# Optimization experiments

Hardware: AMD Instinct MI355X
Metric: run time of the kernel (lower is better)

The kernel has to match this reference:

```python
import jax, jax.numpy as jnp
import numpy as np

B, W, F = 16384, 64, 120
EPS = 1e-3  # keras BatchNormalization default epsilon


def _bn(x, g, b, m, v):
    return g * (x - m) * jax.lax.rsqrt(v + EPS) + b


def setup_inputs() -> dict:
    key = jax.random.key(0)
    ks = jax.random.split(key, 32)
    n = lambda i, s: jax.random.normal(ks[i], s, dtype=jnp.float32) * 0.05
    u = lambda i, s: jax.random.uniform(ks[i], s, dtype=jnp.float32) + 0.5
    W3 = W * 3
    return {
        'x': jax.random.normal(ks[0], (B, W, F), dtype=jnp.float32),
        # per-timestep Conv1D: only center tap matters on length-1 seq -> [W, F, 3]
        'conv_w': n(1, (W, F, 3)), 'conv_b': n(2, (W, 3)),
        # eye head
        'e_g1': u(3, (W3,)), 'e_b1': n(4, (W3,)), 'e_m1': n(5, (W3,)), 'e_v1': u(6, (W3,)),
        'e_d1_w': n(7, (W3, W3)), 'e_d1_b': n(8, (W3,)),
        'e_g2': u(9, (W3,)), 'e_b2': n(10, (W3,)), 'e_m2': n(11, (W3,)), 'e_v2': u(12, (W3,)),
        'e_d2_w': n(13, (W3, 2 * F)), 'e_d2_b': n(14, (2 * F,)),
        'e_d3_w': n(15, (2 * F, F)), 'e_d3_b': n(16, (F,)),
        # blink head
        'b_g1': u(17, (W3,)), 'b_b1': n(18, (W3,)), 'b_m1': n(19, (W3,)), 'b_v1': u(20, (W3,)),
        'b_d1_w': n(21, (W3, W)), 'b_d1_b': n(22, (W,)),
        'b_g2': u(23, (W,)), 'b_b2': n(24, (W,)), 'b_m2': n(25, (W,)), 'b_v2': u(26, (W,)),
        'b_d2_w': n(27, (W, W // 2)), 'b_d2_b': n(28, (W // 2,)),
        'b_d3_w': n(29, (W // 2, 1)), 'b_d3_b': n(30, (1,)),
    }


def reference(x, conv_w, conv_b, e_g1, e_b1, e_m1, e_v1, e_d1_w, e_d1_b,
              e_g2, e_b2, e_m2, e_v2, e_d2_w, e_d2_b, e_d3_w, e_d3_b,
              b_g1, b_b1, b_m1, b_v1, b_d1_w, b_d1_b,
              b_g2, b_b2, b_m2, b_v2, b_d2_w, b_d2_b, b_d3_w, b_d3_b):
    # window_size independent Conv1D(k=3,'same') on length-1 sequences reduce to a
    # single batched per-timestep matmul with the center kernel tap.
    combined = jnp.tanh(jnp.einsum('bwf,wfk->bwk', x, conv_w) + conv_b)
    combined = combined.reshape(x.shape[0], -1)  # [B, 3*W]
    # eye-feature head (dropout = identity at inference, BN uses moving stats)
    e = _bn(combined, e_g1, e_b1, e_m1, e_v1)
    e = jnp.tanh(e @ e_d1_w + e_d1_b)
    e = _bn(e, e_g2, e_b2, e_m2, e_v2)
    e = e @ e_d2_w + e_d2_b
    e = e @ e_d3_w + e_d3_b  # [B, F]
    # blink head
    b = _bn(combined, b_g1, b_b1, b_m1, b_v1)
    b = jnp.tanh(b @ b_d1_w + b_d1_b)
    b = _bn(b, b_g2, b_b2, b_m2, b_v2)
    b = jnp.tanh(b @ b_d2_w + b_d2_b)
    b = jax.nn.sigmoid(b @ b_d3_w + b_d3_b)  # [B, 1]
    return jnp.concatenate([e, b], axis=-1)  # [B, F+1]
```

## Files before the change

kernel.cpp:

```cpp
#include <hip/hip_runtime.h>
#include <hip/hip_bf16.h>
#include <string.h>

#define EPSBN 1e-3f

constexpr int kC1  = 192;
constexpr int kN2  = 240;
constexpr int kOut = 121;
constexpr int BTOT = 16384;

typedef __attribute__((ext_vector_type(8))) short bf16x8;
typedef __attribute__((ext_vector_type(4))) float f32x4;

__device__ __forceinline__ unsigned short f2bf(float f) {
  union { float f; unsigned u; } v; v.f = f;
  unsigned r = v.u + 0x7FFFu + ((v.u >> 16) & 1u);
  return (unsigned short)(r >> 16);
}
__device__ __forceinline__ float bf2f(unsigned short h) {
  union { unsigned u; float f; } v; v.u = ((unsigned)h) << 16;
  return v.f;
}

constexpr size_t OFF_W1E  = 0;
constexpr size_t OFF_W2E  = OFF_W1E + 73728;
constexpr size_t OFF_W3E  = OFF_W2E + 92160;
constexpr size_t OFF_W1B  = OFF_W3E + 65536;
constexpr size_t OFF_W2B  = OFF_W1B + 24576;
constexpr size_t OFF_BIAS = OFF_W2B + 4096;
constexpr size_t OFF_CWT  = OFF_BIAS + 2736;
constexpr size_t WS_NEED  = OFF_CWT + 122880;

__device__ __forceinline__ void pack_one(unsigned short* dst, int idx,
                                         const float* __restrict__ W, int Ksrc, int Nsrc,
                                         int KS, const float* g, const float* v)
{
  int per_nt = KS * 512;
  int nt = idx / per_nt; int r = idx - nt * per_nt;
  int ks = r >> 9; int r2 = r & 511;
  int l = r2 >> 3; int j = r2 & 7;
  int i = ks * 32 + ((l >> 4) << 3) + j;
  int n = (nt << 4) + (l & 15);
  float val = 0.f;
  if (i < Ksrc && n < Nsrc) {
    float s = g ? g[i] * rsqrtf(v[i] + EPSBN) : 1.f;
    val = s * W[(size_t)i * Nsrc + n];
  }
  dst[idx] = f2bf(val);
}

__device__ __forceinline__ float wave_dot192(const float* g, const float* b,
                                             const float* m, const float* vv,
                                             const float* W, int Nsrc, int j, int lane)
{
  float p = 0.f;
  #pragma unroll
  for (int t = 0; t < 3; ++t) {
    int i = t * 64 + lane;
    float s = g[i] * rsqrtf(vv[i] + EPSBN);
    p = fmaf(b[i] - m[i] * s, W[(size_t)i * Nsrc + j], p);
  }
  #pragma unroll
  for (int o = 32; o > 0; o >>= 1) p += __shfl_xor(p, o);
  return p;
}

__global__ __launch_bounds__(256) void prep_all(
    const float* conv_w,
    const float* e_g1, const float* e_b1, const float* e_m1, const float* e_v1,
    const float* e_d1_w, const float* e_d1_b,
    const float* e_g2, const float* e_b2, const float* e_m2, const float* e_v2,
    const float* e_d2_w, const float* e_d2_b,
    const float* e_d3_w, const float* e_d3_b,
    const float* b_g1, const float* b_b1, const float* b_m1, const float* b_v1,
    const float* b_d1_w, const float* b_d1_b,
    const float* b_g2, const float* b_b2, const float* b_m2, const float* b_v2,
    const float* b_d2_w, const float* b_d2_b,
    const float* b_d3_w, const float* b_d3_b,
    unsigned short* W1E, unsigned short* W2E, unsigned short* W3E,
    unsigned short* W1B, unsigned short* W2B,
    float* BIAS, float* cwt4)
{
  const int b   = blockIdx.x;
  const int tid = threadIdx.x;

  if (b < 508) {
    int e = b * 256 + tid;
    if (e < 36864)               pack_one(W1E, e,          e_d1_w, 192, 192, 6, e_g1, e_v1);
    else if (e < 82944)          pack_one(W2E, e - 36864,  e_d2_w, 192, 240, 6, e_g2, e_v2);
    else if (e < 115712)         pack_one(W3E, e - 82944,  e_d3_w, 240, 120, 8, nullptr, nullptr);
    else if (e < 128000)         pack_one(W1B, e - 115712, b_d1_w, 192, 64,  6, b_g1, b_v1);
    else if (e < 130048)         pack_one(W2B, e - 128000, b_d2_w, 64,  32,  2, b_g2, b_v2);
  } else if (b < 538) {
    int idx = (b - 508) * 256 + tid;
    if (idx < 7680) {
      int f = idx >> 6, w = idx & 63;
      float4 v;
      v.x = conv_w[(size_t)w * 360 + f * 3 + 0];
      v.y = conv_w[(size_t)w * 360 + f * 3 + 1];
      v.z = conv_w[(size_t)w * 360 + f * 3 + 2];
      v.w = 0.f;
      *reinterpret_cast<float4*>(cwt4 + (size_t)idx * 4) = v;
    }
  } else {
    int lane = tid & 63;
    int q = (b - 538) * 4 + (tid >> 6);
    if (q > 680) return;
    float r;
    if (q < 192) {
      r = wave_dot192(e_g1, e_b1, e_m1, e_v1, e_d1_w, 192, q, lane) + e_d1_b[q];
    } else if (q < 432) {
      int j = q - 192;
      r = wave_dot192(e_g2, e_b2, e_m2, e_v2, e_d2_w, 240, j, lane) + e_d2_b[j];
    } else if (q < 552) {
      r = e_d3_b[q - 432];
    } else if (q < 616) {
      int j = q - 552;
      r = wave_dot192(b_g1, b_b1, b_m1, b_v1, b_d1_w, 64, j, lane) + b_d1_b[j];
    } else if (q < 648) {
      int j = q - 616;
      float s = b_g2[lane] * rsqrtf(b_v2[lane] + EPSBN);
      float p = (b_b2[lane] - b_m2[lane] * s) * b_d2_w[(size_t)lane * 32 + j];
      #pragma unroll
      for (int o = 32; o > 0; o >>= 1) p += __shfl_xor(p, o);
      r = p + b_d2_b[j];
    } else if (q < 680) {
      r = b_d3_w[q - 648];
    } else {
      r = b_d3_b[0];
    }
    if (lane == 0) BIAS[q] = r;
  }
}

__global__ __launch_bounds__(64) void fused_all(
    const float* __restrict__ x,
    const float* __restrict__ cwt4, const float* __restrict__ conv_b,
    const unsigned short* __restrict__ W1E, const unsigned short* __restrict__ W2E,
    const unsigned short* __restrict__ W3E, const unsigned short* __restrict__ W1B,
    const unsigned short* __restrict__ W2B, const float* __restrict__ BIAS,
    float* __restrict__ out)
{
  __shared__ __align__(16) short Ac[16 * 200];
  __shared__ __align__(16) char  ubuf[15 * 65 * 16];

  float4* xt = reinterpret_cast<float4*>(ubuf);
  short*  Hs = reinterpret_cast<short*>(ubuf);
  short*  H2 = reinterpret_cast<short*>(ubuf + 6400);

  const int l = threadIdx.x;
  const int R = blockIdx.x * 16;

  {
    const float bc0 = conv_b[l * 3 + 0];
    const float bc1 = conv_b[l * 3 + 1];
    const float bc2 = conv_b[l * 3 + 2];

    for (int r = 0; r < 16; ++r) {
      const float* xrow = x + (size_t)(R + r) * 7680;
      float a0 = 0.f, a1 = 0.f, a2 = 0.f;

      for (int h = 0; h < 2; ++h) {
        #pragma unroll
        for (int i = 0; i < 15; ++i) {
          int g = i * 64 + l;
          int w = g / 15, fs = g - 15 * w;
          float4 v = *reinterpret_cast<const float4*>(xrow + w * 120 + h * 60 + 4 * fs);
          xt[fs * 65 + w] = v;
        }
        __syncthreads();

        #pragma unroll 5
        for (int fq = 0; fq < 15; ++fq) {
          float4 x4 = xt[fq * 65 + l];
          float xs[4] = {x4.x, x4.y, x4.z, x4.w};
          #pragma unroll
          for (int j = 0; j < 4; ++j) {
            int f = h * 60 + 4 * fq + j;
            float4 c4 = *reinterpret_cast<const float4*>(cwt4 + (size_t)(f * 64 + l) * 4);
            a0 = fmaf(xs[j], c4.x, a0);
            a1 = fmaf(xs[j], c4.y, a1);
            a2 = fmaf(xs[j], c4.z, a2);
          }
        }
        __syncthreads();
      }

      Ac[r * 200 + 3 * l + 0] = (short)f2bf(tanhf(a0 + bc0));
      Ac[r * 200 + 3 * l + 1] = (short)f2bf(tanhf(a1 + bc1));
      Ac[r * 200 + 3 * l + 2] = (short)f2bf(tanhf(a2 + bc2));
    }
  }
  __syncthreads();

  #pragma unroll
  for (int e = l; e < 256; e += 64) {
    int row = e >> 4, cc = e & 15;
    H2[row * 264 + 240 + cc] = 0;
  }

  const int arow = l & 15;
  const int kofs = (l >> 4) * 8;
  const int mb   = (l >> 4) * 4;

  for (int nt = 0; nt < 12; ++nt) {
    f32x4 acc = {0.f, 0.f, 0.f, 0.f};
    const bf16x8* bp = (const bf16x8*)W1E + (size_t)(nt * 6) * 64 + l;
    #pragma unroll
    for (int ks = 0; ks < 6; ++ks) {
      bf16x8 a = *(const bf16x8*)(Ac + arow * 200 + ks * 32 + kofs);
      acc = __builtin_amdgcn_mfma_f32_16x16x32_bf16(a, bp[(size_t)ks * 64], acc, 0, 0, 0);
    }
    int n = nt * 16 + arow;
    float bv = BIAS[n];
    __syncthreads();
    #pragma unroll
    for (int r = 0; r < 4; ++r)
      Hs[(mb + r) * 200 + n] = (short)f2bf(tanhf(acc[r] + bv));
  }
  __syncthreads();

  for (int nt = 0; nt < 15; ++nt) {
    f32x4 acc = {0.f, 0.f, 0.f, 0.f};
    const bf16x8* bp = (const bf16x8*)W2E + (size_t)(nt * 6) * 64 + l;
    #pragma unroll
    for (int ks = 0; ks < 6; ++ks) {
      bf16x8 a = *(const bf16x8*)(Hs + arow * 200 + ks * 32 + kofs);
      acc = __builtin_amdgcn_mfma_f32_16x16x32_bf16(a, bp[(size_t)ks * 64], acc, 0, 0, 0);
    }
    int n = nt * 16 + arow;
    float bv = BIAS[192 + n];
    #pragma unroll
    for (int r = 0; r < 4; ++r)
      H2[(mb + r) * 264 + n] = (short)f2bf(acc[r] + bv);
  }
  __syncthreads();

  for (int nt = 0; nt < 8; ++nt) {
    f32x4 acc = {0.f, 0.f, 0.f, 0.f};
    const bf16x8* bp = (const bf16x8*)W3E + (size_t)(nt * 8) * 64 + l;
    #pragma unroll
    for (int ks = 0; ks < 8; ++ks) {
      bf16x8 a = *(const bf16x8*)(H2 + arow * 264 + ks * 32 + kofs);
      acc = __builtin_amdgcn_mfma_f32_16x16x32_bf16(a, bp[(size_t)ks * 64], acc, 0, 0, 0);
    }
    int n = nt * 16 + arow;
    if (n < 120) {
      float bv = BIAS[432 + n];
      #pragma unroll
      for (int r = 0; r < 4; ++r)
        out[(size_t)(R + mb + r) * kOut + n] = acc[r] + bv;
    }
  }
  __syncthreads();

  for (int nt = 0; nt < 4; ++nt) {
    f32x4 acc = {0.f, 0.f, 0.f, 0.f};
    const bf16x8* bp = (const bf16x8*)W1B + (size_t)(nt * 6) * 64 + l;
    #pragma unroll
    for (int ks = 0; ks < 6; ++ks) {
      bf16x8 a = *(const bf16x8*)(Ac + arow * 200 + ks * 32 + kofs);
      acc = __builtin_amdgcn_mfma_f32_16x16x32_bf16(a, bp[(size_t)ks * 64], acc, 0, 0, 0);
    }
    int n = nt * 16 + arow;
    float bv = BIAS[552 + n];
    #pragma unroll
    for (int r = 0; r < 4; ++r)
      Hs[(mb + r) * 200 + n] = (short)f2bf(tanhf(acc[r] + bv));
  }
  __syncthreads();

  for (int nt = 0; nt < 2; ++nt) {
    f32x4 acc = {0.f, 0.f, 0.f, 0.f};
    const bf16x8* bp = (const bf16x8*)W2B + (size_t)(nt * 2) * 64 + l;
    #pragma unroll
    for (int ks = 0; ks < 2; ++ks) {
      bf16x8 a = *(const bf16x8*)(Hs + arow * 200 + ks * 32 + kofs);
      acc = __builtin_amdgcn_mfma_f32_16x16x32_bf16(a, bp[(size_t)ks * 64], acc, 0, 0, 0);
    }
    int n = nt * 16 + arow;
    float bv = BIAS[616 + n];
    #pragma unroll
    for (int r = 0; r < 4; ++r)
      H2[(mb + r) * 264 + n] = (short)f2bf(tanhf(acc[r] + bv));
  }
  __syncthreads();

  if (l < 16) {
    float s = BIAS[680];
    #pragma unroll
    for (int i = 0; i < 32; ++i)
      s = fmaf(bf2f((unsigned short)H2[l * 264 + i]), BIAS[648 + i], s);
    out[(size_t)(R + l) * kOut + 120] = 1.f / (1.f + expf(-s));
  }
}

constexpr int CSTR = 193;
__global__ __launch_bounds__(64, 4) void fused_blink_fb(
    const float* __restrict__ x,
    const float* __restrict__ conv_w, const float* __restrict__ conv_b,
    const float* __restrict__ e_g1, const float* __restrict__ e_b1,
    const float* __restrict__ e_m1, const float* __restrict__ e_v1,
    const float* __restrict__ e_d1_w, const float* __restrict__ e_d1_b,
    const float* __restrict__ e_g2, const float* __restrict__ e_b2,
    const float* __restrict__ e_m2, const float* __restrict__ e_v2,
    const float* __restrict__ e_d2_w, const float* __restrict__ e_d2_b,
    const float* __restrict__ e_d3_w, const float* __restrict__ e_d3_b,
    const float* __restrict__ b_g1, const float* __restrict__ b_b1,
    const float* __restrict__ b_m1, const float* __restrict__ b_v1,
    const float* __restrict__ b_d1_w, const float* __restrict__ b_d1_b,
    const float* __restrict__ b_g2, const float* __restrict__ b_b2,
    const float* __restrict__ b_m2, const float* __restrict__ b_v2,
    const float* __restrict__ b_d2_w, const float* __restrict__ b_d2_b,
    const float* __restrict__ b_d3_w, const float* __restrict__ b_d3_b,
    float* __restrict__ out)
{
  __shared__ float comb[4 * CSTR];
  __shared__ __align__(16) float Ab[4 * kN2];
  __shared__ __align__(16) float Bb[4 * kN2];
  const int lane = threadIdx.x;
  const int b0   = blockIdx.x * 4;
  {
    const int rcv = lane >> 4, wloc = lane & 15;
    for (int wc = 0; wc < 4; ++wc) {
      const int w = wc * 16 + wloc;
      const float* xr  = x + ((size_t)(b0 + rcv) * 64 + w) * 120;
      const float* cwp = conv_w + (size_t)w * 360;
      float a0 = 0.f, a1 = 0.f, a2 = 0.f;
      for (int t = 0; t < 30; ++t) {
        float4 xv = *reinterpret_cast<const float4*>(xr + 4 * t);
        float4 c0 = *reinterpret_cast<const float4*>(cwp + 12 * t);
        float4 c1 = *reinterpret_cast<const float4*>(cwp + 12 * t + 4);
        float4 c2 = *reinterpret_cast<const float4*>(cwp + 12 * t + 8);
        a0 += xv.x * c0.x + xv.y * c0.w + xv.z * c1.z + xv.w * c2.y;
        a1 += xv.x * c0.y + xv.y * c1.x + xv.z * c1.w + xv.w * c2.z;
        a2 += xv.x * c0.z + xv.y * c1.y + xv.z * c2.x + xv.w * c2.w;
      }
      comb[rcv * CSTR + 3 * w + 0] = tanhf(a0 + conv_b[3 * w + 0]);
      comb[rcv * CSTR + 3 * w + 1] = tanhf(a1 + conv_b[3 * w + 1]);
      comb[rcv * CSTR + 3 * w + 2] = tanhf(a2 + conv_b[3 * w + 2]);
    }
  }
  __syncthreads();
  #define AR(rr) (Ab + (size_t)(rr) * kN2)
  #define BR(rr) (Bb + (size_t)(rr) * kN2)
  #pragma unroll
  for (int q = 0; q < 12; ++q) {
    int rr = q / 3, cc = q % 3;
    int i = cc * 64 + lane;
    float s = e_g1[i] * rsqrtf(e_v1[i] + EPSBN);
    AR(rr)[i] = comb[rr * CSTR + i] * s + (e_b1[i] - e_m1[i] * s);
  }
  __syncthreads();
  {
    float acc[4][3];
    #pragma unroll
    for (int rr = 0; rr < 4; ++rr) { acc[rr][0]=acc[rr][1]=acc[rr][2]=0.f; }
    for (int i = 0; i < kC1; i += 4) {
      float4 v[4];
      #pragma unroll
      for (int rr = 0; rr < 4; ++rr) v[rr] = *reinterpret_cast<const float4*>(AR(rr) + i);
      #pragma unroll
      for (int io = 0; io < 4; ++io) {
        const float* wp = e_d1_w + (size_t)(i + io) * kC1 + lane;
        float w0 = wp[0], w1 = wp[64], w2 = wp[128];
        #pragma unroll
        for (int rr = 0; rr < 4; ++rr) {
          float xv = reinterpret_cast<const float*>(&v[rr])[io];
          acc[rr][0] = fmaf(xv, w0, acc[rr][0]);
          acc[rr][1] = fmaf(xv, w1, acc[rr][1]);
          acc[rr][2] = fmaf(xv, w2, acc[rr][2]);
        }
      }
    }
    #pragma unroll
    for (int c = 0; c < 3; ++c) {
      int j = c * 64 + lane;
      float s  = e_g2[j] * rsqrtf(e_v2[j] + EPSBN);
      float t  = e_b2[j] - e_m2[j] * s;
      float bs = e_d1_b[j];
      #pragma unroll
      for (int rr = 0; rr < 4; ++rr)
        BR(rr)[j] = tanhf(acc[rr][c] + bs) * s + t;
    }
  }
  __syncthreads();
  {
    const bool m3 = (lane < 48);
    float acc[4][4];
    #pragma unroll
    for (int rr = 0; rr < 4; ++rr) { acc[rr][0]=acc[rr][1]=acc[rr][2]=acc[rr][3]=0.f; }
    for (int i = 0; i < kC1; i += 4) {
      float4 v[4];
      #pragma unroll
      for (int rr = 0; rr < 4; ++rr) v[rr] = *reinterpret_cast<const float4*>(BR(rr) + i);
      #pragma unroll
      for (int io = 0; io < 4; ++io) {
        const float* wp = e_d2_w + (size_t)(i + io) * kN2 + lane;
        float w0 = wp[0], w1 = wp[64], w2 = wp[128];
        float w3 = m3 ? wp[192] : 0.f;
        #pragma unroll
        for (int rr = 0; rr < 4; ++rr) {
          float xv = reinterpret_cast<const float*>(&v[rr])[io];
          acc[rr][0] = fmaf(xv, w0, acc[rr][0]);
          acc[rr][1] = fmaf(xv, w1, acc[rr][1]);
          acc[rr][2] = fmaf(xv, w2, acc[rr][2]);
          acc[rr][3] = fmaf(xv, w3, acc[rr][3]);
        }
      }
    }
    #pragma unroll
    for (int c = 0; c < 4; ++c) {
      int j = c * 64 + lane;
      if (c < 3 || m3) {
        float bs = e_d2_b[j];
        #pragma unroll
        for (int rr = 0; rr < 4; ++rr)
          AR(rr)[j] = acc[rr][c] + bs;
      }
    }
  }
  __syncthreads();
  #pragma unroll
  for (int q = 0; q < 12; ++q) {
    int rr = q / 3, cc = q % 3;
    int i = cc * 64 + lane;
    float s = b_g1[i] * rsqrtf(b_v1[i] + EPSBN);
    BR(rr)[i] = comb[rr * CSTR + i] * s + (b_b1[i] - b_m1[i] * s);
  }
  {
    const bool m56 = (lane < 56);
    float acc[4][2];
    #pragma unroll
    for (int rr = 0; rr < 4; ++rr) { acc[rr][0]=acc[rr][1]=0.f; }
    for (int i = 0; i < kN2; i += 4) {
      float4 v[4];
      #pragma unroll
      for (int rr = 0; rr < 4; ++rr) v[rr] = *reinterpret_cast<const float4*>(AR(rr) + i);
      #pragma unroll
      for (int io = 0; io < 4; ++io) {
        const float* wp = e_d3_w + (size_t)(i + io) * 120 + lane;
        float w0 = wp[0];
        float w1 = m56 ? wp[64] : 0.f;
        #pragma unroll
        for (int rr = 0; rr < 4; ++rr) {
          float xv = reinterpret_cast<const float*>(&v[rr])[io];
          acc[rr][0] = fmaf(xv, w0, acc[rr][0]);
          acc[rr][1] = fmaf(xv, w1, acc[rr][1]);
        }
      }
    }
    #pragma unroll
    for (int c = 0; c < 2; ++c) {
      int j = c * 64 + lane;
      if (j < 120) {
        float bs = e_d3_b[j];
        #pragma unroll
        for (int rr = 0; rr < 4; ++rr)
          out[(size_t)(b0 + rr) * kOut + j] = acc[rr][c] + bs;
      }
    }
  }
  __syncthreads();
  {
    float acc[4] = {0.f, 0.f, 0.f, 0.f};
    for (int i = 0; i < kC1; i += 4) {
      float4 v[4];
      #pragma unroll
      for (int rr = 0; rr < 4; ++rr) v[rr] = *reinterpret_cast<const float4*>(BR(rr) + i);
      #pragma unroll
      for (int io = 0; io < 4; ++io) {
        float w0 = b_d1_w[(size_t)(i + io) * 64 + lane];
        #pragma unroll
        for (int rr = 0; rr < 4; ++rr) {
          float xv = reinterpret_cast<const float*>(&v[rr])[io];
          acc[rr] = fmaf(xv, w0, acc[rr]);
        }
      }
    }
    float s  = b_g2[lane] * rsqrtf(b_v2[lane] + EPSBN);
    float t  = b_b2[lane] - b_m2[lane] * s;
    float bs = b_d1_b[lane];
    #pragma unroll
    for (int rr = 0; rr < 4; ++rr)
      AR(rr)[lane] = tanhf(acc[rr] + bs) * s + t;
  }
  __syncthreads();
  {
    const bool m32 = (lane < 32);
    float acc[4] = {0.f, 0.f, 0.f, 0.f};
    for (int i = 0; i < 64; i += 4) {
      float4 v[4];
      #pragma unroll
      for (int rr = 0; rr < 4; ++rr) v[rr] = *reinterpret_cast<const float4*>(AR(rr) + i);
      #pragma unroll
      for (int io = 0; io < 4; ++io) {
        float w0 = m32 ? b_d2_w[(size_t)(i + io) * 32 + lane] : 0.f;
        #pragma unroll
        for (int rr = 0; rr < 4; ++rr) {
          float xv = reinterpret_cast<const float*>(&v[rr])[io];
          acc[rr] = fmaf(xv, w0, acc[rr]);
        }
      }
    }
    if (m32) {
      float bs = b_d2_b[lane];
      #pragma unroll
      for (int rr = 0; rr < 4; ++rr)
        BR(rr)[lane] = tanhf(acc[rr] + bs);
    }
  }
  __syncthreads();
  if (lane < 4) {
    int rr = lane;
    float acc = b_d3_b[0];
    #pragma unroll
    for (int i = 0; i < 32; ++i)
      acc = fmaf(BR(rr)[i], b_d3_w[i], acc);
    out[(size_t)(b0 + rr) * kOut + 120] = 1.f / (1.f + expf(-acc));
  }
  #undef AR
  #undef BR
}

extern "C" void kernel_launch(void* const* d_in, const int* in_sizes, int n_in,
                              void* d_out, int out_size, void* d_ws, size_t ws_size,
                              hipStream_t stream) {
  (void)in_sizes; (void)n_in; (void)out_size;
  const float* p[31];
  for (int i = 0; i < 31; ++i) p[i] = (const float*)d_in[i];
  float* out = (float*)d_out;

  if (ws_size >= WS_NEED && d_ws != nullptr) {
    char* ws = (char*)d_ws;
    unsigned short* W1E = (unsigned short*)(ws + OFF_W1E);
    unsigned short* W2E = (unsigned short*)(ws + OFF_W2E);
    unsigned short* W3E = (unsigned short*)(ws + OFF_W3E);
    unsigned short* W1B = (unsigned short*)(ws + OFF_W1B);
    unsigned short* W2B = (unsigned short*)(ws + OFF_W2B);
    float* BIAS         = (float*)(ws + OFF_BIAS);
    float* cwt4         = (float*)(ws + OFF_CWT);

    hipLaunchKernelGGL(prep_all, dim3(709), dim3(256), 0, stream,
                       p[1],
                       p[3], p[4], p[5], p[6], p[7], p[8],
                       p[9], p[10], p[11], p[12], p[13], p[14],
                       p[15], p[16],
                       p[17], p[18], p[19], p[20], p[21], p[22],
                       p[23], p[24], p[25], p[26], p[27], p[28],
                       p[29], p[30],
                       W1E, W2E, W3E, W1B, W2B, BIAS, cwt4);
    hipLaunchKernelGGL(fused_all, dim3(BTOT / 16), dim3(64), 0, stream,
                       p[0], cwt4, p[2], W1E, W2E, W3E, W1B, W2B, BIAS, out);
  } else {
    hipLaunchKernelGGL(fused_blink_fb, dim3(BTOT / 4), dim3(64), 0, stream,
      p[0], p[1], p[2], p[3], p[4], p[5], p[6], p[7], p[8], p[9],
      p[10], p[11], p[12], p[13], p[14], p[15], p[16], p[17], p[18], p[19],
      p[20], p[21], p[22], p[23], p[24], p[25], p[26], p[27], p[28], p[29], p[30],
      out);
  }
}
```

Before: 165.7 us.

## Split fused kernel across two waves per block with wave-local conv buffers

```diff
diff --git a/kernel.cpp b/kernel.cpp
--- a/kernel.cpp
+++ b/kernel.cpp
@@ -3,6 +3,10 @@
 #include <string.h>
 
 #define EPSBN 1e-3f
+#define WAVE_FENCE() do { \
+  __asm__ volatile("s_waitcnt lgkmcnt(0)" ::: "memory"); \
+  __builtin_amdgcn_sched_barrier(0); \
+} while (0)
 
 constexpr int kC1  = 192;
 constexpr int kN2  = 240;
@@ -133,7 +137,7 @@
   }
 }
 
-__global__ __launch_bounds__(64) void fused_all(
+__global__ __launch_bounds__(128) void fused_all(
     const float* __restrict__ x,
     const float* __restrict__ cwt4, const float* __restrict__ conv_b,
     const unsigned short* __restrict__ W1E, const unsigned short* __restrict__ W2E,
@@ -142,22 +146,25 @@
     float* __restrict__ out)
 {
   __shared__ __align__(16) short Ac[16 * 200];
-  __shared__ __align__(16) char  ubuf[15 * 65 * 16];
-
-  float4* xt = reinterpret_cast<float4*>(ubuf);
-  short*  Hs = reinterpret_cast<short*>(ubuf);
-  short*  H2 = reinterpret_cast<short*>(ubuf + 6400);
-
-  const int l = threadIdx.x;
-  const int R = blockIdx.x * 16;
+  __shared__ __align__(16) char  ubuf[31200];
+
+  const int tid = threadIdx.x;
+  const int v   = tid >> 6;
+  const int l   = tid & 63;
+  const int R   = blockIdx.x * 16;
+
+  float4* xtv = reinterpret_cast<float4*>(ubuf + v * 15600);
+  short*  Hs  = reinterpret_cast<short*>(ubuf);
+  short*  H2  = reinterpret_cast<short*>(ubuf + 6400);
 
   {
     const float bc0 = conv_b[l * 3 + 0];
     const float bc1 = conv_b[l * 3 + 1];
     const float bc2 = conv_b[l * 3 + 2];
 
-    for (int r = 0; r < 16; ++r) {
-      const float* xrow = x + (size_t)(R + r) * 7680;
+    for (int r = 0; r < 8; ++r) {
+      const int row = 8 * v + r;
+      const float* xrow = x + (size_t)(R + row) * 7680;
       float a0 = 0.f, a1 = 0.f, a2 = 0.f;
 
       for (int h = 0; h < 2; ++h) {
@@ -165,14 +172,14 @@
         for (int i = 0; i < 15; ++i) {
           int g = i * 64 + l;
           int w = g / 15, fs = g - 15 * w;
-          float4 v = *reinterpret_cast<const float4*>(xrow + w * 120 + h * 60 + 4 * fs);
-          xt[fs * 65 + w] = v;
-        }
-        __syncthreads();
+          float4 vv = *reinterpret_cast<const float4*>(xrow + w * 120 + h * 60 + 4 * fs);
+          xtv[fs * 65 + w] = vv;
+        }
+        WAVE_FENCE();
 
         #pragma unroll 5
         for (int fq = 0; fq < 15; ++fq) {
-          float4 x4 = xt[fq * 65 + l];
+          float4 x4 = xtv[fq * 65 + l];
           float xs[4] = {x4.x, x4.y, x4.z, x4.w};
           #pragma unroll
           for (int j = 0; j < 4; ++j) {
@@ -183,27 +190,27 @@
             a2 = fmaf(xs[j], c4.z, a2);
           }
         }
-        __syncthreads();
-      }
-
-      Ac[r * 200 + 3 * l + 0] = (short)f2bf(tanhf(a0 + bc0));
-      Ac[r * 200 + 3 * l + 1] = (short)f2bf(tanhf(a1 + bc1));
-      Ac[r * 200 + 3 * l + 2] = (short)f2bf(tanhf(a2 + bc2));
-    }
-  }
-  __syncthreads();
-
-  #pragma unroll
-  for (int e = l; e < 256; e += 64) {
+        WAVE_FENCE();
+      }
+
+      Ac[row * 200 + 3 * l + 0] = (short)f2bf(tanhf(a0 + bc0));
+      Ac[row * 200 + 3 * l + 1] = (short)f2bf(tanhf(a1 + bc1));
+      Ac[row * 200 + 3 * l + 2] = (short)f2bf(tanhf(a2 + bc2));
+    }
+  }
+  __syncthreads();
+
+  for (int e = tid; e < 256; e += 128) {
     int row = e >> 4, cc = e & 15;
     H2[row * 264 + 240 + cc] = 0;
   }
+  __syncthreads();
 
   const int arow = l & 15;
   const int kofs = (l >> 4) * 8;
   const int mb   = (l >> 4) * 4;
 
-  for (int nt = 0; nt < 12; ++nt) {
+  for (int nt = 6 * v; nt < 6 * v + 6; ++nt) {
     f32x4 acc = {0.f, 0.f, 0.f, 0.f};
     const bf16x8* bp = (const bf16x8*)W1E + (size_t)(nt * 6) * 64 + l;
     #pragma unroll
@@ -213,14 +220,13 @@
     }
     int n = nt * 16 + arow;
     float bv = BIAS[n];
-    __syncthreads();
     #pragma unroll
     for (int r = 0; r < 4; ++r)
       Hs[(mb + r) * 200 + n] = (short)f2bf(tanhf(acc[r] + bv));
   }
   __syncthreads();
 
-  for (int nt = 0; nt < 15; ++nt) {
+  for (int nt = v ? 8 : 0; nt < (v ? 15 : 8); ++nt) {
     f32x4 acc = {0.f, 0.f, 0.f, 0.f};
     const bf16x8* bp = (const bf16x8*)W2E + (size_t)(nt * 6) * 64 + l;
     #pragma unroll
@@ -236,7 +242,7 @@
   }
   __syncthreads();
 
-  for (int nt = 0; nt < 8; ++nt) {
+  for (int nt = 4 * v; nt < 4 * v + 4; ++nt) {
     f32x4 acc = {0.f, 0.f, 0.f, 0.f};
     const bf16x8* bp = (const bf16x8*)W3E + (size_t)(nt * 8) * 64 + l;
     #pragma unroll
@@ -252,9 +258,7 @@
         out[(size_t)(R + mb + r) * kOut + n] = acc[r] + bv;
     }
   }
-  __syncthreads();
-
-  for (int nt = 0; nt < 4; ++nt) {
+  for (int nt = 2 * v; nt < 2 * v + 2; ++nt) {
     f32x4 acc = {0.f, 0.f, 0.f, 0.f};
     const bf16x8* bp = (const bf16x8*)W1B + (size_t)(nt * 6) * 64 + l;
     #pragma unroll
@@ -270,7 +274,8 @@
   }
   __syncthreads();
 
-  for (int nt = 0; nt < 2; ++nt) {
+  {
+    int nt = v;
     f32x4 acc = {0.f, 0.f, 0.f, 0.f};
     const bf16x8* bp = (const bf16x8*)W2B + (size_t)(nt * 2) * 64 + l;
     #pragma unroll
@@ -286,7 +291,7 @@
   }
   __syncthreads();
 
-  if (l < 16) {
+  if (v == 0 && l < 16) {
     float s = BIAS[680];
     #pragma unroll
     for (int i = 0; i < 32; ++i)
@@ -550,7 +555,7 @@
                        p[23], p[24], p[25], p[26], p[27], p[28],
                        p[29], p[30],
                        W1E, W2E, W3E, W1B, W2B, BIAS, cwt4);
-    hipLaunchKernelGGL(fused_all, dim3(BTOT / 16), dim3(64), 0, stream,
+    hipLaunchKernelGGL(fused_all, dim3(BTOT / 16), dim3(128), 0, stream,
                        p[0], cwt4, p[2], W1E, W2E, W3E, W1B, W2B, BIAS, out);
   } else {
     hipLaunchKernelGGL(fused_blink_fb, dim3(BTOT / 4), dim3(64), 0, stream,
```

After: 180.4 us. 8.9% more time.
